# Kernel tuning notes

Measured on AMD Instinct MI355X. Metric: run time of the kernel, lower is better.

Reference implementation:

```python
import jax, jax.numpy as jnp
import numpy as np

N = 2500   # total_neurons
K = 50     # connections_per_neuron
T = 60     # temporal_sequence
F = 5      # input_features
H = 128    # lstm hidden_size
B = 512    # batch
GROUPS = [800, 700, 600, 400]  # support_resistance, trend_detection, pattern_recognition, volume_analysis


def _lstm_layer(x, Wih, Whh, bih, bhh):
    # x: [B, T, D]; PyTorch gate order (i, f, g, o); eval mode (no dropout)
    bs = x.shape[0]
    h0 = jnp.zeros((bs, H), x.dtype)

    def step(carry, xt):
        h, c = carry
        g = xt @ Wih.T + h @ Whh.T + bih + bhh
        i, f, gg, o = jnp.split(g, 4, axis=-1)
        c = jax.nn.sigmoid(f) * c + jax.nn.sigmoid(i) * jnp.tanh(gg)
        h = jax.nn.sigmoid(o) * jnp.tanh(c)
        return (h, c), h

    (h, c), ys = jax.lax.scan(step, (h0, h0), jnp.swapaxes(x, 0, 1))
    return jnp.swapaxes(ys, 0, 1), h


def _forward(x, W_ih0, W_hh0, b_ih0, b_hh0, W_ih1, W_hh1, b_ih1, b_hh1,
             fp_w1, fp_b1, fp_w2, fp_b2, conn_w, sens, thr,
             int_w1, int_b1, int_w2, int_b2, int_w3, int_b3,
             tw, tb, pw, pb, kw, kb, vw, vb, cw, cb, conn_idx):
    y0, _ = _lstm_layer(x, W_ih0, W_hh0, b_ih0, b_hh0)
    _, hlast = _lstm_layer(y0, W_ih1, W_hh1, b_ih1, b_hh1)        # hidden[-1]: [B, H]
    base = jnp.tanh(jax.nn.relu(hlast @ fp_w1.T + fp_b1) @ fp_w2.T + fp_b2)  # [B, 32]
    # all_activations = base repeated over N neurons; each neuron reduces its
    # K gathered activations (weighted) and the identical 32 feature dims to a scalar.
    feat_sum = base.sum(-1)                                        # [B]
    acts = jnp.broadcast_to(feat_sum[:, None], (x.shape[0], N))    # [B, N]
    gathered = acts[:, conn_idx]                                   # [B, N, K] irregular gather
    wi = jnp.einsum('bnk,nk->bn', gathered, conn_w)                # [B, N]
    pre = wi * sens
    o0 = GROUPS[0]; o1 = o0 + GROUPS[1]; o2 = o1 + GROUPS[2]
    neuron_out = jnp.concatenate([
        jax.nn.sigmoid(pre[:, :o0] - thr[:o0]),                    # support_resistance
        jnp.tanh(pre[:, o0:o1]),                                   # trend_detection
        jax.nn.relu(pre[:, o1:o2] - thr[o1:o2]),                   # pattern_recognition
        jax.nn.sigmoid(pre[:, o2:]),                               # volume_analysis
    ], axis=1)                                                     # [B, N]
    h1 = jax.nn.relu(neuron_out @ int_w1.T + int_b1)
    h2 = jax.nn.relu(h1 @ int_w2.T + int_b2)
    integrated = jnp.tanh(h2 @ int_w3.T + int_b3)                  # [B, 32]
    trend = integrated @ tw.T + tb                                 # [B, 3]
    patt = integrated @ pw.T + pb                                  # [B, 6]
    keyl = integrated @ kw.T + kb                                  # [B, 4]
    vol = integrated @ vw.T + vb                                   # [B, 1]
    conf = integrated @ cw.T + cb                                  # [B, 1]
    means = jnp.stack([neuron_out[:, :o0].mean(1), neuron_out[:, o0:o1].mean(1),
                       neuron_out[:, o1:o2].mean(1), neuron_out[:, o2:].mean(1)], axis=-1)
    # heads(15) + raw confidence(1) + overall_confidence(1) + specialty means(4) -> [B, 21]? no: 3+6+4+1+1+1+4 = 20
    return jnp.concatenate([trend, patt, keyl, vol, conf, jax.nn.sigmoid(conf), means], axis=-1)


def setup_inputs() -> dict:
    key = jax.random.key(0)
    ks = jax.random.split(key, 40)
    rn = lambda k, s, sc=0.1: jax.random.normal(k, s, dtype=jnp.float32) * sc
    inp = {}
    inp['x'] = jax.random.normal(ks[0], (B, T, F), dtype=jnp.float32)
    inp['W_ih0'] = rn(ks[1], (4 * H, F)); inp['W_hh0'] = rn(ks[2], (4 * H, H))
    inp['b_ih0'] = rn(ks[3], (4 * H,));   inp['b_hh0'] = rn(ks[4], (4 * H,))
    inp['W_ih1'] = rn(ks[5], (4 * H, H)); inp['W_hh1'] = rn(ks[6], (4 * H, H))
    inp['b_ih1'] = rn(ks[7], (4 * H,));   inp['b_hh1'] = rn(ks[8], (4 * H,))
    inp['fp_w1'] = rn(ks[9], (64, H));    inp['fp_b1'] = rn(ks[10], (64,))
    inp['fp_w2'] = rn(ks[11], (32, 64));  inp['fp_b2'] = rn(ks[12], (32,))
    inp['conn_w'] = rn(ks[13], (N, K))
    inp['sens'] = 1.0 + rn(ks[14], (N,))
    inp['thr'] = 0.6 + rn(ks[15], (N,))
    inp['int_w1'] = rn(ks[16], (256, N), 0.02); inp['int_b1'] = rn(ks[17], (256,))
    inp['int_w2'] = rn(ks[18], (64, 256));      inp['int_b2'] = rn(ks[19], (64,))
    inp['int_w3'] = rn(ks[20], (32, 64));       inp['int_b3'] = rn(ks[21], (32,))
    inp['tw'] = rn(ks[22], (3, 32)); inp['tb'] = rn(ks[23], (3,))
    inp['pw'] = rn(ks[24], (6, 32)); inp['pb'] = rn(ks[25], (6,))
    inp['kw'] = rn(ks[26], (4, 32)); inp['kb'] = rn(ks[27], (4,))
    inp['vw'] = rn(ks[28], (1, 32)); inp['vb'] = rn(ks[29], (1,))
    inp['cw'] = rn(ks[30], (1, 32)); inp['cb'] = rn(ks[31], (1,))
    inp['conn_idx'] = jax.random.randint(ks[32], (N, K), 0, N)
    return inp


def reference(x, W_ih0, W_hh0, b_ih0, b_hh0, W_ih1, W_hh1, b_ih1, b_hh1,
              fp_w1, fp_b1, fp_w2, fp_b2, conn_w, sens, thr,
              int_w1, int_b1, int_w2, int_b2, int_w3, int_b3,
              tw, tb, pw, pb, kw, kb, vw, vb, cw, cb, conn_idx):
    return _forward(x, W_ih0, W_hh0, b_ih0, b_hh0, W_ih1, W_hh1, b_ih1, b_hh1,
                    fp_w1, fp_b1, fp_w2, fp_b2, conn_w, sens, thr,
                    int_w1, int_b1, int_w2, int_b2, int_w3, int_b3,
                    tw, tb, pw, pb, kw, kb, vw, vb, cw, cb, conn_idx)
```

## Files before the change

### kernel.cpp

```cpp
#include <hip/hip_runtime.h>
#include <math.h>

#define NB   512
#define TT   60
#define FF   5
#define HH   128
#define G4   512
#define NN   2500
#define KK   50

#define O0 800
#define O1 1500
#define O2 2100

#define OFF_B0F   0
#define OFF_B1F   40960
#define OFF_BIAS0 106496
#define OFF_BIAS1 107008
#define OFF_A     107520
#define OFF_FS    110020
#define OFF_H1    110532

#define PREP_T0 81920
#define PREP_T1 212992
#define PREP_T2 213504
#define PREP_T3 214016
#define PREP_TOTAL 216516

typedef _Float16 f16x8 __attribute__((ext_vector_type(8)));
typedef float f32x4 __attribute__((ext_vector_type(4)));

#define MFMA16(A, B, C) __builtin_amdgcn_mfma_f32_16x16x32_f16((A), (B), (C), 0, 0, 0)

__device__ __forceinline__ float sigf(float x) {
    return 1.0f / (1.0f + __expf(-x));
}
__device__ __forceinline__ float tanh2(float x) {
    float e = __expf(-2.0f * x);
    return fmaf(2.0f, 1.0f / (1.0f + e), -1.0f);
}

__global__ __launch_bounds__(256) void prep_kernel(
    const float* __restrict__ W_ih0, const float* __restrict__ W_hh0,
    const float* __restrict__ b_ih0, const float* __restrict__ b_hh0,
    const float* __restrict__ W_ih1, const float* __restrict__ W_hh1,
    const float* __restrict__ b_ih1, const float* __restrict__ b_hh1,
    const float* __restrict__ conn_w, const float* __restrict__ sens,
    float* __restrict__ ws)
{
    int i = blockIdx.x * 256 + threadIdx.x;
    if (i >= PREP_TOTAL) return;

    if (i < PREP_T0) {
        int j = i & 7, l = (i >> 3) & 63;
        int rest = i >> 9;
        int g = rest & 3;
        int kbw = rest >> 2;
        int kb = kbw % 5, w = kbw / 5;
        int k = kb * 32 + (l >> 4) * 8 + j;
        int n = g * 128 + w * 16 + (l & 15);
        float val = 0.f;
        if (k < 128)       val = W_hh0[n * HH + k];
        else if (k < 133)  val = W_ih0[n * FF + (k - 128)];
        ((_Float16*)(ws + OFF_B0F))[i] = (_Float16)val;
    } else if (i < PREP_T1) {
        int v = i - PREP_T0;
        int j = v & 7, l = (v >> 3) & 63;
        int rest = v >> 9;
        int g = rest & 3;
        int kb = (rest >> 2) & 7;
        int w = rest >> 5;
        int k = kb * 32 + (l >> 4) * 8 + j;
        int n = g * 128 + w * 16 + (l & 15);
        float val = (k < 128) ? W_ih1[n * HH + k] : W_hh1[n * HH + (k - 128)];
        ((_Float16*)(ws + OFF_B1F))[v] = (_Float16)val;
    } else if (i < PREP_T2) {
        int j = i - PREP_T1;
        ws[OFF_BIAS0 + j] = b_ih0[j] + b_hh0[j];
    } else if (i < PREP_T3) {
        int j = i - PREP_T2;
        ws[OFF_BIAS1 + j] = b_ih1[j] + b_hh1[j];
    } else {
        int n = i - PREP_T3;
        float s = 0.f;
        const float* cw = conn_w + n * KK;
        for (int k = 0; k < KK; ++k) s += cw[k];
        ws[OFF_A + n] = s * sens[n];
    }
}

__global__ __launch_bounds__(512) void lstm_mfma(
    const float* __restrict__ x,
    const float* __restrict__ ws_ro,
    const float* __restrict__ fp_w1, const float* __restrict__ fp_b1,
    const float* __restrict__ fp_w2, const float* __restrict__ fp_b2,
    float* __restrict__ feat_sum)
{
    __shared__ __align__(16) _Float16 hcat[2 * 4096];
    __shared__ _Float16 xsh[16][312];
    __shared__ float t1s[16][65];
    __shared__ float bss[16][33];

    const int tid = threadIdx.x;
    const int w = tid >> 6, l = tid & 63;
    const int u = w * 16 + (l & 15);
    const int row0 = (l >> 4) * 4;
    const int bb = blockIdx.x;

    ((uint4*)hcat)[tid] = make_uint4(0u, 0u, 0u, 0u);

    for (int i = tid; i < 16 * TT * FF; i += 512) {
        int r = i / (TT * FF), c = i % (TT * FF);
        xsh[r][c] = (_Float16)x[(bb * 16 + r) * (TT * FF) + c];
    }

    float bia0[4], bia1[4];
#pragma unroll
    for (int g = 0; g < 4; ++g) {
        bia0[g] = ws_ro[OFF_BIAS0 + g * 128 + u];
        bia1[g] = ws_ro[OFF_BIAS1 + g * 128 + u];
    }
    float c0[4] = {0.f, 0.f, 0.f, 0.f};
    float c1[4] = {0.f, 0.f, 0.f, 0.f};

    const f16x8* B0 = (const f16x8*)(ws_ro + OFF_B0F) + w * 20 * 64 + l;
    const f16x8* B1 = (const f16x8*)(ws_ro + OFF_B1F) + w * 32 * 64 + l;
    const f16x8* HF = (const f16x8*)hcat;

    const int h0base = (u >> 5) * 512 + ((u >> 3) & 3) * 128 + (u & 7);
    const int h1base = h0base + 2048;

    __syncthreads();

    auto step = [&](int SRC, int DST, int t) {
        const f16x8* hs = HF + SRC * 512;
        const f16x8* hd = HF + DST * 512;
        _Float16* hw = hcat + DST * 4096;

        f16x8 xaf = {(_Float16)0, (_Float16)0, (_Float16)0, (_Float16)0,
                     (_Float16)0, (_Float16)0, (_Float16)0, (_Float16)0};
        if (l < 16) {
            const _Float16* xr = &xsh[l][t * FF];
            xaf[0] = xr[0]; xaf[1] = xr[1]; xaf[2] = xr[2];
            xaf[3] = xr[3]; xaf[4] = xr[4];
        }

        f32x4 a0 = {bia0[0], bia0[0], bia0[0], bia0[0]};
        f32x4 a1 = {bia0[1], bia0[1], bia0[1], bia0[1]};
        f32x4 a2 = {bia0[2], bia0[2], bia0[2], bia0[2]};
        f32x4 a3 = {bia0[3], bia0[3], bia0[3], bia0[3]};
#pragma unroll
        for (int kb = 0; kb < 4; ++kb) {
            f16x8 af = hs[kb * 64 + l];
            a0 = MFMA16(af, B0[(kb*4+0)*64], a0);
            a1 = MFMA16(af, B0[(kb*4+1)*64], a1);
            a2 = MFMA16(af, B0[(kb*4+2)*64], a2);
            a3 = MFMA16(af, B0[(kb*4+3)*64], a3);
        }
        a0 = MFMA16(xaf, B0[(16+0)*64], a0);
        a1 = MFMA16(xaf, B0[(16+1)*64], a1);
        a2 = MFMA16(xaf, B0[(16+2)*64], a2);
        a3 = MFMA16(xaf, B0[(16+3)*64], a3);

#pragma unroll
        for (int r = 0; r < 4; ++r) {
            float gi = sigf(a0[r]);
            float gf = sigf(a1[r]);
            float gg = tanh2(a2[r]);
            float go = sigf(a3[r]);
            c0[r] = gf * c0[r] + gi * gg;
            hw[h0base + (row0 + r) * 8] = (_Float16)(go * tanh2(c0[r]));
        }
        __syncthreads();

        f32x4 b0 = {bia1[0], bia1[0], bia1[0], bia1[0]};
        f32x4 b1 = {bia1[1], bia1[1], bia1[1], bia1[1]};
        f32x4 b2 = {bia1[2], bia1[2], bia1[2], bia1[2]};
        f32x4 b3 = {bia1[3], bia1[3], bia1[3], bia1[3]};
#pragma unroll
        for (int kb = 0; kb < 8; ++kb) {
            f16x8 af = (kb < 4) ? hd[kb * 64 + l] : hs[kb * 64 + l];
            b0 = MFMA16(af, B1[(kb*4+0)*64], b0);
            b1 = MFMA16(af, B1[(kb*4+1)*64], b1);
            b2 = MFMA16(af, B1[(kb*4+2)*64], b2);
            b3 = MFMA16(af, B1[(kb*4+3)*64], b3);
        }
#pragma unroll
        for (int r = 0; r < 4; ++r) {
            float gi = sigf(b0[r]);
            float gf = sigf(b1[r]);
            float gg = tanh2(b2[r]);
            float go = sigf(b3[r]);
            c1[r] = gf * c1[r] + gi * gg;
            hw[h1base + (row0 + r) * 8] = (_Float16)(go * tanh2(c1[r]));
        }
        __syncthreads();
    };

    for (int t = 0; t < TT; t += 2) {
        step(0, 1, t);
        step(1, 0, t + 1);
    }

    for (int idx = tid; idx < 16 * 64; idx += 512) {
        int r = idx >> 6, m = idx & 63;
        float acc = fp_b1[m];
        const float* wp = fp_w1 + m * HH;
        for (int k = 0; k < HH; ++k) {
            float hv = (float)hcat[2048 + (k >> 5) * 512 +
                                   (r + ((k >> 3) & 3) * 16) * 8 + (k & 7)];
            acc = fmaf(wp[k], hv, acc);
        }
        t1s[r][m] = fmaxf(acc, 0.f);
    }
    __syncthreads();
    if (tid < 16 * 32) {
        int r = tid >> 5, q = tid & 31;
        float acc = fp_b2[q];
        const float* wp = fp_w2 + q * 64;
        for (int m = 0; m < 64; ++m) acc = fmaf(wp[m], t1s[r][m], acc);
        bss[r][q] = tanh2(acc);
    }
    __syncthreads();
    if (tid < 16) {
        float s = 0.f;
        for (int q = 0; q < 32; ++q) s += bss[tid][q];
        feat_sum[bb * 16 + tid] = s;
    }
}

__device__ __forceinline__ float actn(int n, float pre, float th) {
    if (n < O0)       return sigf(pre - th);
    else if (n < O1)  return tanh2(pre);
    else if (n < O2)  return fmaxf(pre - th, 0.f);
    else              return sigf(pre);
}

__global__ __launch_bounds__(256) void gemm_h1(
    const float* __restrict__ feat_sum,
    const float* __restrict__ aw, const float* __restrict__ thr,
    const float* __restrict__ int_w1,
    const float* __restrict__ int_b1,
    float* __restrict__ h1)
{
    __shared__ float As[32][33];
    __shared__ float Bs[32][33];
    const int b0 = blockIdx.x * 32;
    const int m0 = blockIdx.y * 32;
    const int tid = threadIdx.x;
    const int ty = tid >> 4, tx = tid & 15;
    const int li = tid >> 3;
    const int lj = (tid & 7) * 4;

    const float s_li = feat_sum[b0 + li];

    float acc00 = 0.f, acc01 = 0.f, acc10 = 0.f, acc11 = 0.f;

    for (int k0 = 0; k0 < NN; k0 += 32) {
        float4 av = make_float4(0.f, 0.f, 0.f, 0.f);
        if (k0 + lj < NN) {
            float4 aa = *(const float4*)(aw + k0 + lj);
            float4 tt = *(const float4*)(thr + k0 + lj);
            int n = k0 + lj;
            av.x = actn(n + 0, s_li * aa.x, tt.x);
            av.y = actn(n + 1, s_li * aa.y, tt.y);
            av.z = actn(n + 2, s_li * aa.z, tt.z);
            av.w = actn(n + 3, s_li * aa.w, tt.w);
        }
        As[li][lj + 0] = av.x; As[li][lj + 1] = av.y;
        As[li][lj + 2] = av.z; As[li][lj + 3] = av.w;

        float4 wv = make_float4(0.f, 0.f, 0.f, 0.f);
        if (k0 + lj < NN)
            wv = *(const float4*)(int_w1 + (m0 + li) * NN + k0 + lj);
        Bs[lj + 0][li] = wv.x; Bs[lj + 1][li] = wv.y;
        Bs[lj + 2][li] = wv.z; Bs[lj + 3][li] = wv.w;
        __syncthreads();

#pragma unroll 8
        for (int kk = 0; kk < 32; ++kk) {
            float a0 = As[ty * 2][kk],  a1 = As[ty * 2 + 1][kk];
            float w0 = Bs[kk][tx * 2],  w1 = Bs[kk][tx * 2 + 1];
            acc00 += a0 * w0; acc01 += a0 * w1;
            acc10 += a1 * w0; acc11 += a1 * w1;
        }
        __syncthreads();
    }
    const int bi = b0 + ty * 2, mj = m0 + tx * 2;
    h1[bi * 256 + mj]           = fmaxf(acc00 + int_b1[mj], 0.f);
    h1[bi * 256 + mj + 1]       = fmaxf(acc01 + int_b1[mj + 1], 0.f);
    h1[(bi + 1) * 256 + mj]     = fmaxf(acc10 + int_b1[mj], 0.f);
    h1[(bi + 1) * 256 + mj + 1] = fmaxf(acc11 + int_b1[mj + 1], 0.f);
}

__global__ __launch_bounds__(64) void tail_kernel(
    const float* __restrict__ h1,
    const float* __restrict__ feat_sum,
    const float* __restrict__ aw, const float* __restrict__ thr,
    const float* __restrict__ int_w2, const float* __restrict__ int_b2,
    const float* __restrict__ int_w3, const float* __restrict__ int_b3,
    const float* __restrict__ tw, const float* __restrict__ tb,
    const float* __restrict__ pw, const float* __restrict__ pb,
    const float* __restrict__ kw, const float* __restrict__ kb,
    const float* __restrict__ vw, const float* __restrict__ vb,
    const float* __restrict__ cw, const float* __restrict__ cb,
    float* __restrict__ out)
{
    const int b = blockIdx.x;
    const int lane = threadIdx.x;
    __shared__ float h2s[64];
    __shared__ float ints[32];
    __shared__ float outs[16];
    __shared__ float red[4][64];
    __shared__ float mred[4];

    {
        const float s = feat_sum[b];
        float m0 = 0.f, m1 = 0.f, m2 = 0.f, m3 = 0.f;
        for (int n = lane; n < NN; n += 64) {
            float v = actn(n, s * aw[n], thr[n]);
            if (n < O0) m0 += v; else if (n < O1) m1 += v;
            else if (n < O2) m2 += v; else m3 += v;
        }
        red[0][lane] = m0; red[1][lane] = m1;
        red[2][lane] = m2; red[3][lane] = m3;
    }

    {
        float acc = int_b2[lane];
        const float* hp = h1 + b * 256;
        const float* wp = int_w2 + lane * 256;
        for (int m = 0; m < 256; ++m) acc += wp[m] * hp[m];
        h2s[lane] = fmaxf(acc, 0.f);
    }
    __syncthreads();
    if (lane < 4) {
        float acc = 0.f;
        for (int i = 0; i < 64; ++i) acc += red[lane][i];
        const float inv[4] = {1.f/800.f, 1.f/700.f, 1.f/600.f, 1.f/400.f};
        mred[lane] = acc * inv[lane];
    }
    if (lane < 32) {
        float acc = int_b3[lane];
        const float* wp = int_w3 + lane * 64;
        for (int m = 0; m < 64; ++m) acc += wp[m] * h2s[m];
        ints[lane] = tanh2(acc);
    }
    __syncthreads();
    if (lane < 15) {
        const float* wsel; float bsel;
        if (lane < 3)       { wsel = tw + lane * 32;       bsel = tb[lane]; }
        else if (lane < 9)  { wsel = pw + (lane - 3) * 32; bsel = pb[lane - 3]; }
        else if (lane < 13) { wsel = kw + (lane - 9) * 32; bsel = kb[lane - 9]; }
        else if (lane == 13){ wsel = vw;                   bsel = vb[0]; }
        else                { wsel = cw;                   bsel = cb[0]; }
        float acc = bsel;
        for (int q = 0; q < 32; ++q) acc += wsel[q] * ints[q];
        outs[lane] = acc;
    }
    __syncthreads();
    if (lane < 20) {
        float v;
        if (lane < 15)       v = outs[lane];
        else if (lane == 15) v = sigf(outs[14]);
        else                 v = mred[lane - 16];
        out[b * 20 + lane] = v;
    }
}

extern "C" void kernel_launch(void* const* d_in, const int* in_sizes, int n_in,
                              void* d_out, int out_size, void* d_ws, size_t ws_size,
                              hipStream_t stream)
{
    const float* x      = (const float*)d_in[0];
    const float* W_ih0  = (const float*)d_in[1];
    const float* W_hh0  = (const float*)d_in[2];
    const float* b_ih0  = (const float*)d_in[3];
    const float* b_hh0  = (const float*)d_in[4];
    const float* W_ih1  = (const float*)d_in[5];
    const float* W_hh1  = (const float*)d_in[6];
    const float* b_ih1  = (const float*)d_in[7];
    const float* b_hh1  = (const float*)d_in[8];
    const float* fp_w1  = (const float*)d_in[9];
    const float* fp_b1  = (const float*)d_in[10];
    const float* fp_w2  = (const float*)d_in[11];
    const float* fp_b2  = (const float*)d_in[12];
    const float* conn_w = (const float*)d_in[13];
    const float* sens   = (const float*)d_in[14];
    const float* thr    = (const float*)d_in[15];
    const float* int_w1 = (const float*)d_in[16];
    const float* int_b1 = (const float*)d_in[17];
    const float* int_w2 = (const float*)d_in[18];
    const float* int_b2 = (const float*)d_in[19];
    const float* int_w3 = (const float*)d_in[20];
    const float* int_b3 = (const float*)d_in[21];
    const float* tw     = (const float*)d_in[22];
    const float* tb     = (const float*)d_in[23];
    const float* pw     = (const float*)d_in[24];
    const float* pb     = (const float*)d_in[25];
    const float* kw     = (const float*)d_in[26];
    const float* kb     = (const float*)d_in[27];
    const float* vw     = (const float*)d_in[28];
    const float* vb     = (const float*)d_in[29];
    const float* cw     = (const float*)d_in[30];
    const float* cb     = (const float*)d_in[31];

    float* ws = (float*)d_ws;
    float* out = (float*)d_out;

    prep_kernel<<<(PREP_TOTAL + 255) / 256, 256, 0, stream>>>(
        W_ih0, W_hh0, b_ih0, b_hh0, W_ih1, W_hh1, b_ih1, b_hh1,
        conn_w, sens, ws);

    lstm_mfma<<<NB / 16, 512, 0, stream>>>(
        x, ws, fp_w1, fp_b1, fp_w2, fp_b2, ws + OFF_FS);

    {
        dim3 grid(NB / 32, 256 / 32);
        gemm_h1<<<grid, 256, 0, stream>>>(
            ws + OFF_FS, ws + OFF_A, thr, int_w1, int_b1, ws + OFF_H1);
    }

    tail_kernel<<<NB, 64, 0, stream>>>(
        ws + OFF_H1, ws + OFF_FS, ws + OFF_A, thr,
        int_w2, int_b2, int_w3, int_b3,
        tw, tb, pw, pb, kw, kb, vw, vb, cw, cb,
        out);
}
```

Measured before the change: 451.7 us.

## Materialize neuron activations in a separate kernel and single-buffer LSTM hidden state

A new neuron_kernel computes the per-batch neuron activations and group means once, writing a 512x2500 activation matrix to workspace. gemm_h1 then reads that matrix instead of recomputing the transcendental activations per tile, and tail_kernel reads the precomputed means. The LSTM hidden state goes from double buffering to a single buffer, which needs extra barriers before each write. The trade is a ~5MB global write and read plus one more launch, and twice as many __syncthreads per timestep in the recurrent kernel.

```diff
diff --git a/kernel.cpp b/kernel.cpp
--- a/kernel.cpp
+++ b/kernel.cpp
@@ -19,12 +19,14 @@
 #define OFF_BIAS1 107008
 #define OFF_A     107520
 #define OFF_FS    110020
-#define OFF_H1    110532
-
-#define PREP_T0 81920
-#define PREP_T1 212992
-#define PREP_T2 213504
-#define PREP_T3 214016
+#define OFF_NO    110532
+#define OFF_MEANS 1390532
+#define OFF_H1    1392580
+
+#define P0 81920
+#define P1 212992
+#define P2 213504
+#define P3 214016
 #define PREP_TOTAL 216516
 
 typedef _Float16 f16x8 __attribute__((ext_vector_type(8)));
@@ -51,7 +53,7 @@
     int i = blockIdx.x * 256 + threadIdx.x;
     if (i >= PREP_TOTAL) return;
 
-    if (i < PREP_T0) {
+    if (i < P0) {
         int j = i & 7, l = (i >> 3) & 63;
         int rest = i >> 9;
         int g = rest & 3;
@@ -63,8 +65,8 @@
         if (k < 128)       val = W_hh0[n * HH + k];
         else if (k < 133)  val = W_ih0[n * FF + (k - 128)];
         ((_Float16*)(ws + OFF_B0F))[i] = (_Float16)val;
-    } else if (i < PREP_T1) {
-        int v = i - PREP_T0;
+    } else if (i < P1) {
+        int v = i - P0;
         int j = v & 7, l = (v >> 3) & 63;
         int rest = v >> 9;
         int g = rest & 3;
@@ -74,14 +76,14 @@
         int n = g * 128 + w * 16 + (l & 15);
         float val = (k < 128) ? W_ih1[n * HH + k] : W_hh1[n * HH + (k - 128)];
         ((_Float16*)(ws + OFF_B1F))[v] = (_Float16)val;
-    } else if (i < PREP_T2) {
-        int j = i - PREP_T1;
+    } else if (i < P2) {
+        int j = i - P1;
         ws[OFF_BIAS0 + j] = b_ih0[j] + b_hh0[j];
-    } else if (i < PREP_T3) {
-        int j = i - PREP_T2;
+    } else if (i < P3) {
+        int j = i - P2;
         ws[OFF_BIAS1 + j] = b_ih1[j] + b_hh1[j];
     } else {
-        int n = i - PREP_T3;
+        int n = i - P3;
         float s = 0.f;
         const float* cw = conn_w + n * KK;
         for (int k = 0; k < KK; ++k) s += cw[k];
@@ -96,8 +98,8 @@
     const float* __restrict__ fp_w2, const float* __restrict__ fp_b2,
     float* __restrict__ feat_sum)
 {
-    __shared__ __align__(16) _Float16 hcat[2 * 4096];
-    __shared__ _Float16 xsh[16][312];
+    __shared__ __align__(16) _Float16 hcat[8 * 512];
+    __shared__ _Float16 xsh[16][304];
     __shared__ float t1s[16][65];
     __shared__ float bss[16][33];
 
@@ -132,11 +134,7 @@
 
     __syncthreads();
 
-    auto step = [&](int SRC, int DST, int t) {
-        const f16x8* hs = HF + SRC * 512;
-        const f16x8* hd = HF + DST * 512;
-        _Float16* hw = hcat + DST * 4096;
-
+    for (int t = 0; t < TT; ++t) {
         f16x8 xaf = {(_Float16)0, (_Float16)0, (_Float16)0, (_Float16)0,
                      (_Float16)0, (_Float16)0, (_Float16)0, (_Float16)0};
         if (l < 16) {
@@ -151,7 +149,7 @@
         f32x4 a3 = {bia0[3], bia0[3], bia0[3], bia0[3]};
 #pragma unroll
         for (int kb = 0; kb < 4; ++kb) {
-            f16x8 af = hs[kb * 64 + l];
+            f16x8 af = HF[kb * 64 + l];
             a0 = MFMA16(af, B0[(kb*4+0)*64], a0);
             a1 = MFMA16(af, B0[(kb*4+1)*64], a1);
             a2 = MFMA16(af, B0[(kb*4+2)*64], a2);
@@ -162,6 +160,7 @@
         a2 = MFMA16(xaf, B0[(16+2)*64], a2);
         a3 = MFMA16(xaf, B0[(16+3)*64], a3);
 
+        float h0v[4];
 #pragma unroll
         for (int r = 0; r < 4; ++r) {
             float gi = sigf(a0[r]);
@@ -169,8 +168,12 @@
             float gg = tanh2(a2[r]);
             float go = sigf(a3[r]);
             c0[r] = gf * c0[r] + gi * gg;
-            hw[h0base + (row0 + r) * 8] = (_Float16)(go * tanh2(c0[r]));
-        }
+            h0v[r] = go * tanh2(c0[r]);
+        }
+        __syncthreads();
+#pragma unroll
+        for (int r = 0; r < 4; ++r)
+            hcat[h0base + (row0 + r) * 8] = (_Float16)h0v[r];
         __syncthreads();
 
         f32x4 b0 = {bia1[0], bia1[0], bia1[0], bia1[0]};
@@ -179,12 +182,13 @@
         f32x4 b3 = {bia1[3], bia1[3], bia1[3], bia1[3]};
 #pragma unroll
         for (int kb = 0; kb < 8; ++kb) {
-            f16x8 af = (kb < 4) ? hd[kb * 64 + l] : hs[kb * 64 + l];
+            f16x8 af = HF[kb * 64 + l];
             b0 = MFMA16(af, B1[(kb*4+0)*64], b0);
             b1 = MFMA16(af, B1[(kb*4+1)*64], b1);
             b2 = MFMA16(af, B1[(kb*4+2)*64], b2);
             b3 = MFMA16(af, B1[(kb*4+3)*64], b3);
         }
+        float h1v[4];
 #pragma unroll
         for (int r = 0; r < 4; ++r) {
             float gi = sigf(b0[r]);
@@ -192,14 +196,13 @@
             float gg = tanh2(b2[r]);
             float go = sigf(b3[r]);
             c1[r] = gf * c1[r] + gi * gg;
-            hw[h1base + (row0 + r) * 8] = (_Float16)(go * tanh2(c1[r]));
-        }
-        __syncthreads();
-    };
-
-    for (int t = 0; t < TT; t += 2) {
-        step(0, 1, t);
-        step(1, 0, t + 1);
+            h1v[r] = go * tanh2(c1[r]);
+        }
+        __syncthreads();
+#pragma unroll
+        for (int r = 0; r < 4; ++r)
+            hcat[h1base + (row0 + r) * 8] = (_Float16)h1v[r];
+        __syncthreads();
     }
 
     for (int idx = tid; idx < 16 * 64; idx += 512) {
@@ -236,9 +239,34 @@
     else              return sigf(pre);
 }
 
+__global__ __launch_bounds__(256) void neuron_kernel(
+    const float* __restrict__ feat_sum, const float* __restrict__ a,
+    const float* __restrict__ thr,
+    float* __restrict__ no, float* __restrict__ means)
+{
+    const int b = blockIdx.x;
+    const float s = feat_sum[b];
+    float g0 = 0.f, g1 = 0.f, g2 = 0.f, g3 = 0.f;
+    for (int n = threadIdx.x; n < NN; n += 256) {
+        float v = actn(n, s * a[n], thr[n]);
+        if (n < O0) g0 += v; else if (n < O1) g1 += v;
+        else if (n < O2) g2 += v; else g3 += v;
+        no[b * NN + n] = v;
+    }
+    __shared__ float red[4][256];
+    red[0][threadIdx.x] = g0; red[1][threadIdx.x] = g1;
+    red[2][threadIdx.x] = g2; red[3][threadIdx.x] = g3;
+    __syncthreads();
+    if (threadIdx.x < 4) {
+        float acc = 0.f;
+        for (int i = 0; i < 256; ++i) acc += red[threadIdx.x][i];
+        const float inv[4] = {1.f/800.f, 1.f/700.f, 1.f/600.f, 1.f/400.f};
+        means[b * 4 + threadIdx.x] = acc * inv[threadIdx.x];
+    }
+}
+
 __global__ __launch_bounds__(256) void gemm_h1(
-    const float* __restrict__ feat_sum,
-    const float* __restrict__ aw, const float* __restrict__ thr,
+    const float* __restrict__ no,
     const float* __restrict__ int_w1,
     const float* __restrict__ int_b1,
     float* __restrict__ h1)
@@ -252,21 +280,12 @@
     const int li = tid >> 3;
     const int lj = (tid & 7) * 4;
 
-    const float s_li = feat_sum[b0 + li];
-
     float acc00 = 0.f, acc01 = 0.f, acc10 = 0.f, acc11 = 0.f;
 
     for (int k0 = 0; k0 < NN; k0 += 32) {
         float4 av = make_float4(0.f, 0.f, 0.f, 0.f);
-        if (k0 + lj < NN) {
-            float4 aa = *(const float4*)(aw + k0 + lj);
-            float4 tt = *(const float4*)(thr + k0 + lj);
-            int n = k0 + lj;
-            av.x = actn(n + 0, s_li * aa.x, tt.x);
-            av.y = actn(n + 1, s_li * aa.y, tt.y);
-            av.z = actn(n + 2, s_li * aa.z, tt.z);
-            av.w = actn(n + 3, s_li * aa.w, tt.w);
-        }
+        if (k0 + lj < NN)
+            av = *(const float4*)(no + (b0 + li) * NN + k0 + lj);
         As[li][lj + 0] = av.x; As[li][lj + 1] = av.y;
         As[li][lj + 2] = av.z; As[li][lj + 3] = av.w;
 
@@ -295,8 +314,6 @@
 
 __global__ __launch_bounds__(64) void tail_kernel(
     const float* __restrict__ h1,
-    const float* __restrict__ feat_sum,
-    const float* __restrict__ aw, const float* __restrict__ thr,
     const float* __restrict__ int_w2, const float* __restrict__ int_b2,
     const float* __restrict__ int_w3, const float* __restrict__ int_b3,
     const float* __restrict__ tw, const float* __restrict__ tb,
@@ -304,6 +321,7 @@
     const float* __restrict__ kw, const float* __restrict__ kb,
     const float* __restrict__ vw, const float* __restrict__ vb,
     const float* __restrict__ cw, const float* __restrict__ cb,
+    const float* __restrict__ means,
     float* __restrict__ out)
 {
     const int b = blockIdx.x;
@@ -311,20 +329,6 @@
     __shared__ float h2s[64];
     __shared__ float ints[32];
     __shared__ float outs[16];
-    __shared__ float red[4][64];
-    __shared__ float mred[4];
-
-    {
-        const float s = feat_sum[b];
-        float m0 = 0.f, m1 = 0.f, m2 = 0.f, m3 = 0.f;
-        for (int n = lane; n < NN; n += 64) {
-            float v = actn(n, s * aw[n], thr[n]);
-            if (n < O0) m0 += v; else if (n < O1) m1 += v;
-            else if (n < O2) m2 += v; else m3 += v;
-        }
-        red[0][lane] = m0; red[1][lane] = m1;
-        red[2][lane] = m2; red[3][lane] = m3;
-    }
 
     {
         float acc = int_b2[lane];
@@ -334,12 +338,6 @@
         h2s[lane] = fmaxf(acc, 0.f);
     }
     __syncthreads();
-    if (lane < 4) {
-        float acc = 0.f;
-        for (int i = 0; i < 64; ++i) acc += red[lane][i];
-        const float inv[4] = {1.f/800.f, 1.f/700.f, 1.f/600.f, 1.f/400.f};
-        mred[lane] = acc * inv[lane];
-    }
     if (lane < 32) {
         float acc = int_b3[lane];
         const float* wp = int_w3 + lane * 64;
@@ -363,7 +361,7 @@
         float v;
         if (lane < 15)       v = outs[lane];
         else if (lane == 15) v = sigf(outs[14]);
-        else                 v = mred[lane - 16];
+        else                 v = means[b * 4 + (lane - 16)];
         out[b * 20 + lane] = v;
     }
 }
@@ -415,15 +413,17 @@
     lstm_mfma<<<NB / 16, 512, 0, stream>>>(
         x, ws, fp_w1, fp_b1, fp_w2, fp_b2, ws + OFF_FS);
 
+    neuron_kernel<<<NB, 256, 0, stream>>>(
+        ws + OFF_FS, ws + OFF_A, thr, ws + OFF_NO, ws + OFF_MEANS);
+
     {
         dim3 grid(NB / 32, 256 / 32);
         gemm_h1<<<grid, 256, 0, stream>>>(
-            ws + OFF_FS, ws + OFF_A, thr, int_w1, int_b1, ws + OFF_H1);
+            ws + OFF_NO, int_w1, int_b1, ws + OFF_H1);
     }
 
     tail_kernel<<<NB, 64, 0, stream>>>(
-        ws + OFF_H1, ws + OFF_FS, ws + OFF_A, thr,
-        int_w2, int_b2, int_w3, int_b3,
+        ws + OFF_H1, int_w2, int_b2, int_w3, int_b3,
         tw, tb, pw, pb, kw, kb, vw, vb, cw, cb,
-        out);
-}
+        ws + OFF_MEANS, out);
+}
```

Measured after the change: 437.1 us. -3.2%, faster.
